# Kernel tuning notes

Measured on AMD Instinct MI355X. Metric: run time of the kernel, lower is better.

## Reference

```python
import jax, jax.numpy as jnp
import numpy as np

N = 50000
E = 1000000
WIDTH = 64
DEPTH = 4


def setup_inputs() -> dict:
    key = jax.random.key(0)
    ks = jax.random.split(key, 6)
    x = jax.random.normal(ks[0], (N, 5), dtype=jnp.float32)
    edge_index = jax.random.randint(ks[1], (2, E), 0, N, dtype=jnp.int32)
    edge_attr = jax.random.normal(ks[2], (E, 3), dtype=jnp.float32)
    w1 = jax.random.normal(ks[3], (3, WIDTH), dtype=jnp.float32) / jnp.sqrt(3.0)
    b1 = jnp.zeros((WIDTH,), jnp.float32)
    w2 = jax.random.normal(ks[4], (WIDTH, 1), dtype=jnp.float32) / jnp.sqrt(float(WIDTH))
    b2 = jnp.zeros((1,), jnp.float32)
    root = jax.random.normal(ks[5], (1, 1), dtype=jnp.float32)
    bias = jnp.zeros((1,), jnp.float32)
    return dict(x=x, edge_index=edge_index, edge_attr=edge_attr,
                w1=w1, b1=b1, w2=w2, b2=b2, root=root, bias=bias)


def reference(x, edge_index, edge_attr, w1, b1, w2, b2, root, bias):
    # h: scalar node feature, column 2 of data.x -> [N, 1]
    h = x[:, 2:3]
    src, dst = edge_index[0], edge_index[1]  # messages flow src -> dst

    # Per-edge 1x1 weight from the edge MLP (depends only on edge_attr,
    # identical for all depth iterations since the conv is shared).
    w_e = jax.nn.relu(edge_attr @ w1 + b1) @ w2 + b2  # [E, 1]

    # Mean aggregation: precompute in-degree of each target node.
    deg = jax.ops.segment_sum(jnp.ones((E,), jnp.float32), dst, num_segments=N)
    inv_deg = jnp.where(deg > 0, 1.0 / jnp.maximum(deg, 1.0), 0.0)[:, None]  # [N, 1]

    for _ in range(DEPTH):
        msg = h[src] * w_e                                        # gather + per-edge weight, [E, 1]
        agg = jax.ops.segment_sum(msg, dst, num_segments=N) * inv_deg  # scatter-mean, [N, 1]
        h = jax.nn.relu(agg + h @ root + bias)                    # root transform + bias + ReLU
    return h
```

## Files before the change

### kernel.cpp

```cpp
#include <hip/hip_runtime.h>

#define NN 50000
#define NNP 50176
#define NE 1000000
#define NBK 196
#define ESTRIDE 5632
#define EPB3 5120

#define EPB 1024
#define PB 977

__global__ __launch_bounds__(1024)
void place3(const float* __restrict__ x,
            const float* __restrict__ ea,
            const int* __restrict__ src,
            const int* __restrict__ dst,
            const float* __restrict__ w1,
            const float* __restrict__ b1,
            const float* __restrict__ w2,
            const float* __restrict__ b2,
            uint2* __restrict__ es,
            int* __restrict__ cursor,
            float* __restrict__ hA) {
    __shared__ float sw1[192];
    __shared__ float sb1[64];
    __shared__ float sw2[64];
    __shared__ int hist[NBK];
    __shared__ int hbase[NBK];
    const int t = threadIdx.x;
    const int j = blockIdx.x;
    if (t < 192) sw1[t] = w1[t];
    if (t < 64) { sb1[t] = b1[t]; sw2[t] = w2[t]; }
    if (t < NBK) hist[t] = 0;
    {
        int i = j * 1024 + t;
        if (i < NN) hA[i] = x[5 * i + 2];
    }
    __syncthreads();
    const float bz = b2[0];

    float ce[5];
    int dd[5], rr[5], ss[5];
#pragma unroll
    for (int k = 0; k < 5; ++k) {
        int e = j * EPB3 + k * 1024 + t;
        dd[k] = -1;
        if (e < NE) {
            float a0 = ea[3 * e + 0];
            float a1 = ea[3 * e + 1];
            float a2 = ea[3 * e + 2];
            float c0 = bz, c1 = 0.f, c2 = 0.f, c3 = 0.f;
#pragma unroll
            for (int kk = 0; kk < 64; kk += 4) {
                float h0 = fmaf(a0, sw1[kk+0], fmaf(a1, sw1[64+kk+0], fmaf(a2, sw1[128+kk+0], sb1[kk+0])));
                float h1 = fmaf(a0, sw1[kk+1], fmaf(a1, sw1[64+kk+1], fmaf(a2, sw1[128+kk+1], sb1[kk+1])));
                float h2 = fmaf(a0, sw1[kk+2], fmaf(a1, sw1[64+kk+2], fmaf(a2, sw1[128+kk+2], sb1[kk+2])));
                float h3 = fmaf(a0, sw1[kk+3], fmaf(a1, sw1[64+kk+3], fmaf(a2, sw1[128+kk+3], sb1[kk+3])));
                c0 = fmaf(fmaxf(h0, 0.f), sw2[kk+0], c0);
                c1 = fmaf(fmaxf(h1, 0.f), sw2[kk+1], c1);
                c2 = fmaf(fmaxf(h2, 0.f), sw2[kk+2], c2);
                c3 = fmaf(fmaxf(h3, 0.f), sw2[kk+3], c3);
            }
            ce[k] = (c0 + c1) + (c2 + c3);
            ss[k] = src[e];
            int d = dst[e];
            dd[k] = d;
            rr[k] = atomicAdd(&hist[d >> 8], 1);
        }
    }
    __syncthreads();
    if (t < NBK) {
        int hv = hist[t];
        hbase[t] = hv ? atomicAdd(&cursor[t], hv) : 0;
    }
    __syncthreads();
#pragma unroll
    for (int k = 0; k < 5; ++k) {
        if (dd[k] >= 0) {
            int d = dd[k];
            int b = d >> 8;
            int prel = hbase[b] + rr[k];
            int pos = (prel < ESTRIDE) ? (b * ESTRIDE + prel)
                                       : (NBK * ESTRIDE + (t & 63));
            es[pos] = make_uint2((unsigned)ss[k] | ((unsigned)(d & 255) << 17),
                                 __float_as_uint(ce[k]));
        }
    }
}

__global__ __launch_bounds__(1024)
void reorder_csr(const int* __restrict__ cursor,
                 const uint2* __restrict__ es,
                 uint2* __restrict__ es2,
                 uint2* __restrict__ nodePtr) {
    __shared__ int hist[256];
    __shared__ int part[256];
    __shared__ int cur[256];
    const int t = threadIdx.x;
    const int b = blockIdx.x;
    if (t < 256) hist[t] = 0;
    __syncthreads();
    const int s0 = b * ESTRIDE;
    int cnt = cursor[b];
    if (cnt > ESTRIDE) cnt = ESTRIDE;

    uint2 v[6]; int key[6]; bool m[6];
#pragma unroll
    for (int k = 0; k < 6; ++k) {
        int p = k * 1024 + t;
        m[k] = (p < cnt);
        if (m[k]) {
            v[k] = es[s0 + p];
            key[k] = (v[k].x >> 17) & 255;
            atomicAdd(&hist[key[k]], 1);
        }
    }
    __syncthreads();
    int val = 0;
    if (t < 256) { val = hist[t]; part[t] = val; }
    __syncthreads();
    for (int off = 1; off < 256; off <<= 1) {
        int xv = 0, add = 0;
        if (t < 256) { xv = part[t]; if (t >= off) add = part[t - off]; }
        __syncthreads();
        if (t < 256) part[t] = xv + add;
        __syncthreads();
    }
    if (t < 256) {
        int excl = part[t] - val;
        cur[t] = excl;
        nodePtr[b * 256 + t] = make_uint2((unsigned)(s0 + excl), (unsigned)val);
    }
    __syncthreads();
#pragma unroll
    for (int k = 0; k < 6; ++k) {
        if (m[k]) {
            int pos = atomicAdd(&cur[key[k]], 1);
            es2[s0 + pos] = v[k];
        }
    }
}

__global__ __launch_bounds__(256)
void round_csr(const uint2* __restrict__ nodePtr,
               const uint2* __restrict__ es2,
               const float* __restrict__ hold,
               float* __restrict__ hnew,
               const float* __restrict__ root,
               const float* __restrict__ bias) {
    int g = blockIdx.x * 256 + threadIdx.x;
    int row = g >> 3;
    int sub = g & 7;
    uint2 pk = nodePtr[row];
    int beg = (int)pk.x;
    int len = (int)pk.y;
    float acc = 0.f;
    for (int k = sub; k < len; k += 8) {
        uint2 v = es2[beg + k];
        acc += hold[v.x & 0x1FFFF] * __uint_as_float(v.y);
    }
    acc += __shfl_xor(acc, 1);
    acc += __shfl_xor(acc, 2);
    acc += __shfl_xor(acc, 4);
    if (sub == 0 && row < NN) {
        float inv = (len > 0) ? (1.0f / (float)len) : 0.f;
        hnew[row] = fmaxf(fmaf(hold[row], root[0], fmaf(acc, inv, bias[0])), 0.f);
    }
}

__global__ void bucket_count(const int* __restrict__ dst, int* __restrict__ bcnt,
                             const float* __restrict__ x, float* __restrict__ h) {
    __shared__ int hist[NBK];
    int t = threadIdx.x;
    if (t < NBK) hist[t] = 0;
    __syncthreads();
    int gid = blockIdx.x * 256 + t;
    if (gid < NN) h[gid] = x[5 * gid + 2];
#pragma unroll
    for (int j = 0; j < 4; ++j) {
        int e = blockIdx.x * EPB + j * 256 + t;
        if (e < NE) atomicAdd(&hist[dst[e] >> 8], 1);
    }
    __syncthreads();
    if (t < NBK && hist[t]) atomicAdd(&bcnt[t], hist[t]);
}

__global__ void bucket_scan(const int* __restrict__ bcnt,
                            int* __restrict__ sBeg,
                            int* __restrict__ cursor,
                            int* __restrict__ sLim) {
    __shared__ int part[256];
    int t = threadIdx.x;
    int v = (t < NBK) ? ((bcnt[t] + 1) & ~1) : 0;
    part[t] = v;
    __syncthreads();
    for (int off = 1; off < 256; off <<= 1) {
        int x = part[t];
        int add = (t >= off) ? part[t - off] : 0;
        __syncthreads();
        part[t] = x + add;
        __syncthreads();
    }
    if (t < NBK) {
        int excl = part[t] - v;
        sBeg[t] = excl;
        cursor[t] = excl;
        sLim[t] = 0x7FFFFFFF;
    }
}

__global__ void place_kernel(const float* __restrict__ ea,
                             const int* __restrict__ src,
                             const int* __restrict__ dst,
                             const float* __restrict__ w1,
                             const float* __restrict__ b1,
                             const float* __restrict__ w2,
                             const float* __restrict__ b2,
                             const int* __restrict__ sLim,
                             int* __restrict__ cursor,
                             uint2* __restrict__ es,
                             int dumpbase) {
    __shared__ float sw1[192];
    __shared__ float sb1[64];
    __shared__ float sw2[64];
    __shared__ float sce[EPB];
    __shared__ int hist[NBK];
    __shared__ int hbase[NBK];
    int t = threadIdx.x;
    if (t < 192) sw1[t] = w1[t];
    if (t < 64) { sb1[t] = b1[t]; sw2[t] = w2[t]; }
    if (t < NBK) hist[t] = 0;
    __syncthreads();

    int r[4], dd[4];
#pragma unroll
    for (int j = 0; j < 4; ++j) {
        int e = blockIdx.x * EPB + j * 256 + t;
        dd[j] = -1;
        if (e < NE) {
            float a0 = ea[3 * e + 0];
            float a1 = ea[3 * e + 1];
            float a2 = ea[3 * e + 2];
            float c0 = b2[0], c1 = 0.f, c2 = 0.f, c3 = 0.f;
#pragma unroll
            for (int k = 0; k < 64; k += 4) {
                float h0 = fmaf(a0, sw1[k+0], fmaf(a1, sw1[64+k+0], fmaf(a2, sw1[128+k+0], sb1[k+0])));
                float h1 = fmaf(a0, sw1[k+1], fmaf(a1, sw1[64+k+1], fmaf(a2, sw1[128+k+1], sb1[k+1])));
                float h2 = fmaf(a0, sw1[k+2], fmaf(a1, sw1[64+k+2], fmaf(a2, sw1[128+k+2], sb1[k+2])));
                float h3 = fmaf(a0, sw1[k+3], fmaf(a1, sw1[64+k+3], fmaf(a2, sw1[128+k+3], sb1[k+3])));
                c0 = fmaf(fmaxf(h0, 0.f), sw2[k+0], c0);
                c1 = fmaf(fmaxf(h1, 0.f), sw2[k+1], c1);
                c2 = fmaf(fmaxf(h2, 0.f), sw2[k+2], c2);
                c3 = fmaf(fmaxf(h3, 0.f), sw2[k+3], c3);
            }
            sce[j * 256 + t] = (c0 + c1) + (c2 + c3);
            int d = dst[e];
            dd[j] = d;
            r[j] = atomicAdd(&hist[d >> 8], 1);
        }
    }
    __syncthreads();
    if (t < NBK) { int hv = hist[t]; if (hv) hbase[t] = atomicAdd(&cursor[t], hv); }
    __syncthreads();
#pragma unroll
    for (int j = 0; j < 4; ++j) {
        int e = blockIdx.x * EPB + j * 256 + t;
        if (e < NE) {
            int d = dd[j];
            int b = d >> 8;
            int pos = hbase[b] + r[j];
            if (pos >= sLim[b]) pos = dumpbase + (t & 63);
            unsigned pack = (unsigned)src[e] | ((unsigned)(d & 255) << 17);
            es[pos] = make_uint2(pack, __float_as_uint(sce[j * 256 + t]));
        }
    }
}

template<int FIRST>
__global__ __launch_bounds__(1024)
void round_fused_fb(const int* __restrict__ sBeg,
                    const int* __restrict__ sEnd,
                    const int* __restrict__ sLim,
                    const uint2* __restrict__ es,
                    const float* __restrict__ hold,
                    float* __restrict__ hnew,
                    float* __restrict__ invdeg,
                    const float* __restrict__ root,
                    const float* __restrict__ bias) {
    __shared__ float lagg[256];
    __shared__ int ldeg[256];
    int t = threadIdx.x;
    int b = blockIdx.x;
    if (t < 256) { lagg[t] = 0.f; if (FIRST) ldeg[t] = 0; }
    __syncthreads();
    int s0 = sBeg[b];
    int s1 = sEnd[b];
    { int cap = sLim[b]; if (s1 > cap) s1 = cap; }
    const uint4* es4 = (const uint4*)es;
    for (int p = s0 + t * 2; p < s1; p += 2048) {
        uint4 v = es4[p >> 1];
        {
            int sidx = v.x & 0x1FFFF;
            int dl = (v.x >> 17) & 255;
            atomicAdd(&lagg[dl], hold[sidx] * __uint_as_float(v.y));
            if (FIRST) atomicAdd(&ldeg[dl], 1);
        }
        if (p + 1 < s1) {
            int sidx = v.z & 0x1FFFF;
            int dl = (v.z >> 17) & 255;
            atomicAdd(&lagg[dl], hold[sidx] * __uint_as_float(v.w));
            if (FIRST) atomicAdd(&ldeg[dl], 1);
        }
    }
    __syncthreads();
    if (t < 256) {
        int node = b * 256 + t;
        if (node < NN) {
            float inv;
            if (FIRST) {
                int d = ldeg[t];
                inv = (d > 0) ? (1.0f / (float)d) : 0.f;
                invdeg[node] = inv;
            } else {
                inv = invdeg[node];
            }
            hnew[node] = fmaxf(fmaf(hold[node], root[0], fmaf(lagg[t], inv, bias[0])), 0.f);
        }
    }
}


extern "C" void kernel_launch(void* const* d_in, const int* in_sizes, int n_in,
                              void* d_out, int out_size, void* d_ws, size_t ws_size,
                              hipStream_t stream) {
    const float* x    = (const float*)d_in[0];
    const int*   ei   = (const int*)d_in[1];
    const float* ea   = (const float*)d_in[2];
    const float* w1   = (const float*)d_in[3];
    const float* b1   = (const float*)d_in[4];
    const float* w2   = (const float*)d_in[5];
    const float* b2   = (const float*)d_in[6];
    const float* root = (const float*)d_in[7];
    const float* bias = (const float*)d_in[8];

    const int* src = ei;
    const int* dst = ei + NE;
    float* out = (float*)d_out;

    const size_t esN = (size_t)NBK * ESTRIDE + 64;
    const size_t needFixed = esN * 8
                           + (size_t)NBK * ESTRIDE * 8
                           + (size_t)NNP * 8
                           + (size_t)NBK * 4
                           + (size_t)NN * 4 * 2;

    if (ws_size >= needFixed) {
        uint2* es      = (uint2*)d_ws;
        uint2* es2     = es + esN;
        uint2* nodePtr = es2 + (size_t)NBK * ESTRIDE;
        int*   cursor  = (int*)(nodePtr + NNP);
        float* hA      = (float*)(cursor + NBK);
        float* hB      = hA + NN;

        hipMemsetAsync(cursor, 0, NBK * 4, stream);
        place3<<<NBK, 1024, 0, stream>>>(x, ea, src, dst, w1, b1, w2, b2,
                                         es, cursor, hA);
        reorder_csr<<<NBK, 1024, 0, stream>>>(cursor, es, es2, nodePtr);
        const int gR = NNP * 8 / 256;
        round_csr<<<gR, 256, 0, stream>>>(nodePtr, es2, hA, hB, root, bias);
        round_csr<<<gR, 256, 0, stream>>>(nodePtr, es2, hB, hA, root, bias);
        round_csr<<<gR, 256, 0, stream>>>(nodePtr, es2, hA, hB, root, bias);
        round_csr<<<gR, 256, 0, stream>>>(nodePtr, es2, hB, out, root, bias);
    } else {
        uint2* es     = (uint2*)d_ws;
        int*   bcnt   = (int*)(es + NE + NBK);
        int*   cursor = bcnt + NBK;
        int*   sBeg   = cursor + NBK;
        int*   sLim   = sBeg + NBK;
        float* invdeg = (float*)(sLim + NBK);
        float* hB     = invdeg + NN;
        float* h      = out;

        hipMemsetAsync(bcnt, 0, NBK * 4, stream);
        bucket_count<<<PB, 256, 0, stream>>>(dst, bcnt, x, h);
        bucket_scan<<<1, 256, 0, stream>>>(bcnt, sBeg, cursor, sLim);
        place_kernel<<<PB, 256, 0, stream>>>(ea, src, dst, w1, b1, w2, b2,
                                             sLim, cursor, es, 0);
        round_fused_fb<1><<<NBK, 1024, 0, stream>>>(sBeg, cursor, sLim, es, h,  hB, invdeg, root, bias);
        round_fused_fb<0><<<NBK, 1024, 0, stream>>>(sBeg, cursor, sLim, es, hB, h,  invdeg, root, bias);
        round_fused_fb<0><<<NBK, 1024, 0, stream>>>(sBeg, cursor, sLim, es, h,  hB, invdeg, root, bias);
        round_fused_fb<0><<<NBK, 1024, 0, stream>>>(sBeg, cursor, sLim, es, hB, h,  invdeg, root, bias);
    }
}
```

Before: 143.6 us.

## Replace global atomic bucketing with per-block LDS sort and fuse first round into reorder

The placement kernel now sorts each block's edges by bucket in LDS and writes them contiguously, publishing per-block bucket offsets and counts in a table. This replaces the global atomic cursor and the memset. The reorder kernel gathers each bucket's segments from all blocks using a binary search over the prefix sums. It also computes the first message-passing round with LDS float atomics, which removes one round kernel launch. The cost is a binary search per loaded edge, scattered reads across 196 source segments, and a float-atomic accumulation order that differs from the CSR rounds.

```diff
diff --git a/kernel.cpp b/kernel.cpp
--- a/kernel.cpp
+++ b/kernel.cpp
@@ -5,13 +5,13 @@
 #define NE 1000000
 #define NBK 196
 #define ESTRIDE 5632
-#define EPB3 5120
+#define EPB4 5120
 
 #define EPB 1024
 #define PB 977
 
 __global__ __launch_bounds__(1024)
-void place3(const float* __restrict__ x,
+void place4(const float* __restrict__ x,
             const float* __restrict__ ea,
             const int* __restrict__ src,
             const int* __restrict__ dst,
@@ -20,13 +20,15 @@
             const float* __restrict__ w2,
             const float* __restrict__ b2,
             uint2* __restrict__ es,
-            int* __restrict__ cursor,
+            int* __restrict__ ebase,
             float* __restrict__ hA) {
     __shared__ float sw1[192];
     __shared__ float sb1[64];
     __shared__ float sw2[64];
     __shared__ int hist[NBK];
-    __shared__ int hbase[NBK];
+    __shared__ int part[256];
+    __shared__ int lexcl[NBK];
+    __shared__ uint2 eLDS[EPB4];
     const int t = threadIdx.x;
     const int j = blockIdx.x;
     if (t < 192) sw1[t] = w1[t];
@@ -38,14 +40,17 @@
     }
     __syncthreads();
     const float bz = b2[0];
+    const int e0 = j * EPB4;
+    const int myN = (NE - e0 < EPB4) ? (NE - e0) : EPB4;
 
     float ce[5];
     int dd[5], rr[5], ss[5];
 #pragma unroll
     for (int k = 0; k < 5; ++k) {
-        int e = j * EPB3 + k * 1024 + t;
+        int p = k * 1024 + t;
         dd[k] = -1;
-        if (e < NE) {
+        if (p < myN) {
+            int e = e0 + p;
             float a0 = ea[3 * e + 0];
             float a1 = ea[3 * e + 1];
             float a2 = ea[3 * e + 2];
@@ -69,55 +74,61 @@
         }
     }
     __syncthreads();
+    int val = 0;
+    if (t < 256) { val = (t < NBK) ? hist[t] : 0; part[t] = val; }
+    __syncthreads();
+    for (int off = 1; off < 256; off <<= 1) {
+        int xv = 0, add = 0;
+        if (t < 256) { xv = part[t]; if (t >= off) add = part[t - off]; }
+        __syncthreads();
+        if (t < 256) part[t] = xv + add;
+        __syncthreads();
+    }
     if (t < NBK) {
-        int hv = hist[t];
-        hbase[t] = hv ? atomicAdd(&cursor[t], hv) : 0;
+        int excl = part[t] - val;
+        lexcl[t] = excl;
+        ebase[j * NBK + t] = (excl << 16) | val;
     }
     __syncthreads();
 #pragma unroll
     for (int k = 0; k < 5; ++k) {
         if (dd[k] >= 0) {
             int d = dd[k];
-            int b = d >> 8;
-            int prel = hbase[b] + rr[k];
-            int pos = (prel < ESTRIDE) ? (b * ESTRIDE + prel)
-                                       : (NBK * ESTRIDE + (t & 63));
-            es[pos] = make_uint2((unsigned)ss[k] | ((unsigned)(d & 255) << 17),
-                                 __float_as_uint(ce[k]));
-        }
-    }
+            int pos = lexcl[d >> 8] + rr[k];
+            eLDS[pos] = make_uint2((unsigned)ss[k] | ((unsigned)(d & 255) << 17),
+                                   __float_as_uint(ce[k]));
+        }
+    }
+    __syncthreads();
+    for (int p = t; p < myN; p += 1024)
+        es[e0 + p] = eLDS[p];
 }
 
 __global__ __launch_bounds__(1024)
-void reorder_csr(const int* __restrict__ cursor,
-                 const uint2* __restrict__ es,
-                 uint2* __restrict__ es2,
-                 uint2* __restrict__ nodePtr) {
+void sortround1(const int* __restrict__ ebase,
+                const uint2* __restrict__ es,
+                uint2* __restrict__ es2,
+                uint2* __restrict__ nodePtr,
+                const float* __restrict__ hold,
+                float* __restrict__ hnew,
+                const float* __restrict__ root,
+                const float* __restrict__ bias) {
+    __shared__ int cbase[NBK + 1];
+    __shared__ int cex[NBK];
     __shared__ int hist[256];
     __shared__ int part[256];
     __shared__ int cur[256];
+    __shared__ float lagg[256];
     const int t = threadIdx.x;
     const int b = blockIdx.x;
-    if (t < 256) hist[t] = 0;
-    __syncthreads();
-    const int s0 = b * ESTRIDE;
-    int cnt = cursor[b];
-    if (cnt > ESTRIDE) cnt = ESTRIDE;
-
-    uint2 v[6]; int key[6]; bool m[6];
-#pragma unroll
-    for (int k = 0; k < 6; ++k) {
-        int p = k * 1024 + t;
-        m[k] = (p < cnt);
-        if (m[k]) {
-            v[k] = es[s0 + p];
-            key[k] = (v[k].x >> 17) & 255;
-            atomicAdd(&hist[key[k]], 1);
-        }
-    }
-    __syncthreads();
-    int val = 0;
-    if (t < 256) { val = hist[t]; part[t] = val; }
+    if (t < 256) { hist[t] = 0; lagg[t] = 0.f; }
+    int c = 0;
+    if (t < NBK) {
+        int pk = ebase[t * NBK + b];
+        cex[t] = pk >> 16;
+        c = pk & 0xFFFF;
+    }
+    if (t < 256) part[t] = (t < NBK) ? c : 0;
     __syncthreads();
     for (int off = 1; off < 256; off <<= 1) {
         int xv = 0, add = 0;
@@ -126,17 +137,56 @@
         if (t < 256) part[t] = xv + add;
         __syncthreads();
     }
+    if (t < NBK) cbase[t] = part[t] - c;
+    if (t == 0) cbase[NBK] = part[NBK - 1];
+    __syncthreads();
+    const int C = cbase[NBK];
+
+    uint2 v[6]; int key[6]; bool m[6];
+#pragma unroll
+    for (int k = 0; k < 6; ++k) {
+        int p = k * 1024 + t;
+        m[k] = (p < C);
+        if (m[k]) {
+            int lo = 0, hi = NBK - 1;
+            while (lo < hi) { int mid = (lo + hi + 1) >> 1; if (cbase[mid] <= p) lo = mid; else hi = mid - 1; }
+            v[k] = es[lo * EPB4 + cex[lo] + (p - cbase[lo])];
+            key[k] = (v[k].x >> 17) & 255;
+            atomicAdd(&hist[key[k]], 1);
+        }
+    }
+    __syncthreads();
+    int val = 0;
+    if (t < 256) { val = hist[t]; part[t] = val; }
+    __syncthreads();
+    for (int off = 1; off < 256; off <<= 1) {
+        int xv = 0, add = 0;
+        if (t < 256) { xv = part[t]; if (t >= off) add = part[t - off]; }
+        __syncthreads();
+        if (t < 256) part[t] = xv + add;
+        __syncthreads();
+    }
     if (t < 256) {
         int excl = part[t] - val;
         cur[t] = excl;
-        nodePtr[b * 256 + t] = make_uint2((unsigned)(s0 + excl), (unsigned)val);
+        int ec = (excl < ESTRIDE) ? excl : ESTRIDE;
+        nodePtr[b * 256 + t] = make_uint2((unsigned)(b * ESTRIDE + ec), (unsigned)val);
     }
     __syncthreads();
 #pragma unroll
     for (int k = 0; k < 6; ++k) {
         if (m[k]) {
             int pos = atomicAdd(&cur[key[k]], 1);
-            es2[s0 + pos] = v[k];
+            if (pos < ESTRIDE) es2[b * ESTRIDE + pos] = v[k];
+            atomicAdd(&lagg[key[k]], hold[v[k].x & 0x1FFFF] * __uint_as_float(v[k].y));
+        }
+    }
+    __syncthreads();
+    if (t < 256) {
+        int node = b * 256 + t;
+        if (node < NN) {
+            float inv = (val > 0) ? (1.0f / (float)val) : 0.f;
+            hnew[node] = fmaxf(fmaf(hold[node], root[0], fmaf(lagg[t], inv, bias[0])), 0.f);
         }
     }
 }
@@ -347,27 +397,26 @@
     const int* dst = ei + NE;
     float* out = (float*)d_out;
 
-    const size_t esN = (size_t)NBK * ESTRIDE + 64;
-    const size_t needFixed = esN * 8
-                           + (size_t)NBK * ESTRIDE * 8
+    const size_t esN  = (size_t)NBK * EPB4;
+    const size_t es2N = (size_t)NBK * ESTRIDE + 64;
+    const size_t needFixed = esN * 8 + es2N * 8
+                           + (size_t)(NBK * NBK) * 4
                            + (size_t)NNP * 8
-                           + (size_t)NBK * 4
                            + (size_t)NN * 4 * 2;
 
     if (ws_size >= needFixed) {
         uint2* es      = (uint2*)d_ws;
         uint2* es2     = es + esN;
-        uint2* nodePtr = es2 + (size_t)NBK * ESTRIDE;
-        int*   cursor  = (int*)(nodePtr + NNP);
-        float* hA      = (float*)(cursor + NBK);
+        int*   ebase   = (int*)(es2 + es2N);
+        uint2* nodePtr = (uint2*)(ebase + NBK * NBK);
+        float* hA      = (float*)(nodePtr + NNP);
         float* hB      = hA + NN;
 
-        hipMemsetAsync(cursor, 0, NBK * 4, stream);
-        place3<<<NBK, 1024, 0, stream>>>(x, ea, src, dst, w1, b1, w2, b2,
-                                         es, cursor, hA);
-        reorder_csr<<<NBK, 1024, 0, stream>>>(cursor, es, es2, nodePtr);
+        place4<<<NBK, 1024, 0, stream>>>(x, ea, src, dst, w1, b1, w2, b2,
+                                         es, ebase, hA);
+        sortround1<<<NBK, 1024, 0, stream>>>(ebase, es, es2, nodePtr,
+                                             hA, hB, root, bias);
         const int gR = NNP * 8 / 256;
-        round_csr<<<gR, 256, 0, stream>>>(nodePtr, es2, hA, hB, root, bias);
         round_csr<<<gR, 256, 0, stream>>>(nodePtr, es2, hB, hA, root, bias);
         round_csr<<<gR, 256, 0, stream>>>(nodePtr, es2, hA, hB, root, bias);
         round_csr<<<gR, 256, 0, stream>>>(nodePtr, es2, hB, out, root, bias);
```

Measured after the change: 138.4 us. -3.6%, faster.
